# Optimization experiments

Measured on AMD Instinct MI355X. Metric: run time of the kernel, lower is better.

Reference implementation:

```python
import jax, jax.numpy as jnp
import numpy as np

D_IN, D_OUT, RANK = 4096, 4096, 16
ALPHA = 1.0


def setup_inputs() -> dict:
    key = jax.random.key(0)
    ks = jax.random.split(key, 7)
    x = jax.random.normal(ks[0], (8, 2048, D_IN), dtype=jnp.float32)
    W = jax.random.normal(ks[1], (D_IN, D_OUT), dtype=jnp.float32) * (1.0 / np.sqrt(D_IN))
    bias = jax.random.normal(ks[2], (D_OUT,), dtype=jnp.float32) * 0.02
    # he_normal init for a factors; b factors are zeros in the layer, but use small
    # random values so the adapter path contributes numerically to the test.
    a0 = jax.random.normal(ks[3], (D_IN, RANK), dtype=jnp.float32) * np.sqrt(2.0 / D_IN)
    b0 = jax.random.normal(ks[4], (RANK, D_OUT), dtype=jnp.float32) * 0.02
    a1 = jax.random.normal(ks[5], (D_IN, RANK), dtype=jnp.float32) * np.sqrt(2.0 / D_IN)
    b1 = jax.random.normal(ks[6], (RANK, D_OUT), dtype=jnp.float32) * 0.02
    return {"x": x, "W": W, "bias": bias, "a0": a0, "b0": b0, "a1": a1, "b1": b1}


def reference(x, W, bias, a0, b0, a1, b1):
    # LoHA kernel: base + Hadamard product of scaled low-rank factors
    scale = ALPHA / RANK
    p0 = scale * (a0 @ b0)            # [d_in, d_out]
    p1 = scale * (a1 @ b1)            # [d_in, d_out]
    kernel = W + p0 * p1              # [d_in, d_out]
    # Dense call: x @ kernel + bias
    return jnp.einsum('bsd,de->bse', x, kernel) + bias
```

## Files before the change

kernel.cpp:

```cpp
#include <hip/hip_runtime.h>


#define D_IN   4096
#define D_OUT  4096
#define RANKR  16
#define MROWS  16384

typedef __attribute__((ext_vector_type(8))) short short8;
typedef __attribute__((ext_vector_type(4))) float floatx4;

__device__ __forceinline__ unsigned short f2bf(float f) {
    union { float f; unsigned u; } c; c.f = f;
    unsigned r = c.u + 0x7fffu + ((c.u >> 16) & 1u);
    return (unsigned short)(r >> 16);
}

__device__ __forceinline__ void glds16(const void* g, void* l) {
    __builtin_amdgcn_global_load_lds(
        (const __attribute__((address_space(1))) void*)g,
        (__attribute__((address_space(3))) void*)l, 16, 0, 0);
}

__global__ __launch_bounds__(256) void prep(
    const float* __restrict__ W,  const float* __restrict__ a0,
    const float* __restrict__ b0, const float* __restrict__ a1,
    const float* __restrict__ b1, unsigned short* __restrict__ Bt,
    const float* __restrict__ x,  unsigned short* __restrict__ xb) {
    const int tid = threadIdx.x;
    if (blockIdx.x >= 4096) {
        size_t i = ((size_t)(blockIdx.x - 4096) * 256 + tid) * 8;
        const float4* p = (const float4*)(x + i);
        float4 v0 = p[0], v1 = p[1];
        union { unsigned short u[8]; uint4 q; } o;
        o.u[0] = f2bf(v0.x); o.u[1] = f2bf(v0.y);
        o.u[2] = f2bf(v0.z); o.u[3] = f2bf(v0.w);
        o.u[4] = f2bf(v1.x); o.u[5] = f2bf(v1.y);
        o.u[6] = f2bf(v1.z); o.u[7] = f2bf(v1.w);
        *(uint4*)(xb + i) = o.q;
        return;
    }
    __shared__ float Wt[64][65];
    __shared__ float a0t[64][17], a1t[64][17];
    __shared__ float b0t[16][64], b1t[16][64];
    const int k0 = (blockIdx.x & 63) * 64, n0 = (blockIdx.x >> 6) * 64;

    #pragma unroll
    for (int i = 0; i < 16; ++i) {
        int e = i * 256 + tid;
        int kk = e >> 6, nn = e & 63;
        Wt[kk][nn] = W[(size_t)(k0 + kk) * D_OUT + n0 + nn];
    }
    #pragma unroll
    for (int i = 0; i < 4; ++i) {
        int e = i * 256 + tid;
        int kk = e >> 4, r = e & 15;
        a0t[kk][r] = a0[(k0 + kk) * RANKR + r];
        a1t[kk][r] = a1[(k0 + kk) * RANKR + r];
    }
    #pragma unroll
    for (int i = 0; i < 4; ++i) {
        int e = i * 256 + tid;
        int r = e >> 6, nn = e & 63;
        b0t[r][nn] = b0[(size_t)r * D_OUT + n0 + nn];
        b1t[r][nn] = b1[(size_t)r * D_OUT + n0 + nn];
    }
    __syncthreads();

    const float s = 1.0f / 16.0f;
    #pragma unroll 4
    for (int i = 0; i < 16; ++i) {
        int e = i * 256 + tid;
        int kk = e & 63, nn = e >> 6;
        float d0 = 0.f, d1 = 0.f;
        #pragma unroll
        for (int r = 0; r < RANKR; ++r) {
            d0 += a0t[kk][r] * b0t[r][nn];
            d1 += a1t[kk][r] * b1t[r][nn];
        }
        float v = Wt[kk][nn] + (s * d0) * (s * d1);
        Bt[(size_t)(n0 + nn) * D_IN + k0 + kk] = f2bf(v);
    }
}

__global__ __launch_bounds__(256) void gemm_bt(
    const unsigned short* __restrict__ A,
    const unsigned short* __restrict__ B,
    const float* __restrict__ bias,
    float* __restrict__ C) {
    __shared__ __align__(16) unsigned short As[128 * 32];
    __shared__ __align__(16) unsigned short Bs[128 * 32];

    const int tid  = threadIdx.x;
    const int wave = tid >> 6, lane = tid & 63;
    const int quad = lane >> 4, l16 = lane & 15;
    const int m0 = blockIdx.y * 128, n0 = blockIdx.x * 128;
    const int wm = (wave >> 1) * 64, wn = (wave & 1) * 64;
    const int swz = l16 >> 2;

    const unsigned short* Ag = A + (size_t)m0 * D_IN;
    const unsigned short* Bg = B + (size_t)n0 * D_IN;

    floatx4 acc[4][4] = {};

    for (int kt = 0; kt < D_IN; kt += 32) {
        #pragma unroll
        for (int p = 0; p < 2; ++p) {
            int t   = p * 256 + tid;
            int row = t >> 2;
            int cc  = ((t & 3) ^ ((row >> 2) & 3)) * 8;
            unsigned ldsoff = (unsigned)(p * 4096 + wave * 1024);
            glds16(Ag + (size_t)row * D_IN + kt + cc, (char*)As + ldsoff);
            glds16(Bg + (size_t)row * D_IN + kt + cc, (char*)Bs + ldsoff);
        }
        __syncthreads();

        short8 af[4], bf[4];
        #pragma unroll
        for (int mt = 0; mt < 4; ++mt)
            af[mt] = *(const short8*)(As + (wm + mt * 16 + l16) * 32 + (quad ^ swz) * 8);
        #pragma unroll
        for (int nt = 0; nt < 4; ++nt)
            bf[nt] = *(const short8*)(Bs + (wn + nt * 16 + l16) * 32 + (quad ^ swz) * 8);
        #pragma unroll
        for (int mt = 0; mt < 4; ++mt)
            #pragma unroll
            for (int nt = 0; nt < 4; ++nt)
                acc[mt][nt] = __builtin_amdgcn_mfma_f32_16x16x32_bf16(
                    af[mt], bf[nt], acc[mt][nt], 0, 0, 0);
        __syncthreads();
    }

    #pragma unroll
    for (int nt = 0; nt < 4; ++nt) {
        int col = n0 + wn + nt * 16 + l16;
        float bv = bias[col];
        #pragma unroll
        for (int mt = 0; mt < 4; ++mt) {
            int r0 = m0 + wm + mt * 16 + quad * 4;
            #pragma unroll
            for (int r = 0; r < 4; ++r) {
                float v = acc[mt][nt][r] + bv;
                __builtin_nontemporal_store(v, &C[(size_t)(r0 + r) * D_OUT + col]);
            }
        }
    }
}

extern "C" void kernel_launch(void* const* d_in, const int* in_sizes, int n_in,
                              void* d_out, int out_size, void* d_ws, size_t ws_size,
                              hipStream_t stream) {
    const float* x    = (const float*)d_in[0];
    const float* W    = (const float*)d_in[1];
    const float* bias = (const float*)d_in[2];
    const float* a0   = (const float*)d_in[3];
    const float* b0   = (const float*)d_in[4];
    const float* a1   = (const float*)d_in[5];
    const float* b1   = (const float*)d_in[6];
    float* out = (float*)d_out;

    unsigned short* xb = (unsigned short*)d_ws;
    unsigned short* Bt = (unsigned short*)((char*)d_ws + (size_t)MROWS * D_IN * 2);

    prep<<<4096 + (MROWS * (size_t)D_IN) / 2048, 256, 0, stream>>>(
        W, a0, b0, a1, b1, Bt, x, xb);
    gemm_bt<<<dim3(D_OUT / 128, MROWS / 128), 256, 0, stream>>>(xb, Bt, bias, out);
}
```

Before: 1.093 ms.

## Pipeline GEMM with 4-stage LDS ring, 256x256 tiles, and split prep kernels

Rewrites the bf16 GEMM to use 256x256 block tiles with 512 threads, a 4-deep LDS ring buffer fed by async global-to-LDS loads issued three tiles ahead, explicit vmcnt waits, and a single barrier per k-step. It also adds s_setprio around MFMA bursts and a block-index swizzle for L2 locality. The prep kernel is split into a separate x-conversion kernel and a LoHA weight kernel that keeps the a factors in registers and reads b from a transposed LDS layout. The aim is to hide global load latency, raise arithmetic intensity, and cut barrier stalls. The cost is a much larger LDS footprint and more register pressure, which limits occupancy.

```diff
diff --git a/kernel.cpp b/kernel.cpp
--- a/kernel.cpp
+++ b/kernel.cpp
@@ -5,6 +5,7 @@
 #define D_OUT  4096
 #define RANKR  16
 #define MROWS  16384
+#define NTK    128
 
 typedef __attribute__((ext_vector_type(8))) short short8;
 typedef __attribute__((ext_vector_type(4))) float floatx4;
@@ -21,27 +22,26 @@
         (__attribute__((address_space(3))) void*)l, 16, 0, 0);
 }
 
-__global__ __launch_bounds__(256) void prep(
+__global__ __launch_bounds__(256) void cvt_x(const float* __restrict__ x,
+                                             unsigned short* __restrict__ xb) {
+    size_t i = ((size_t)blockIdx.x * 256 + threadIdx.x) * 8;
+    const float4* p = (const float4*)(x + i);
+    float4 v0 = p[0], v1 = p[1];
+    union { unsigned short u[8]; uint4 q; } o;
+    o.u[0] = f2bf(v0.x); o.u[1] = f2bf(v0.y);
+    o.u[2] = f2bf(v0.z); o.u[3] = f2bf(v0.w);
+    o.u[4] = f2bf(v1.x); o.u[5] = f2bf(v1.y);
+    o.u[6] = f2bf(v1.z); o.u[7] = f2bf(v1.w);
+    *(uint4*)(xb + i) = o.q;
+}
+
+__global__ __launch_bounds__(256) void prep_bt(
     const float* __restrict__ W,  const float* __restrict__ a0,
     const float* __restrict__ b0, const float* __restrict__ a1,
-    const float* __restrict__ b1, unsigned short* __restrict__ Bt,
-    const float* __restrict__ x,  unsigned short* __restrict__ xb) {
+    const float* __restrict__ b1, unsigned short* __restrict__ Bt) {
+    __shared__ float Wt[64][65];
+    __shared__ float b0t[64][20], b1t[64][20];
     const int tid = threadIdx.x;
-    if (blockIdx.x >= 4096) {
-        size_t i = ((size_t)(blockIdx.x - 4096) * 256 + tid) * 8;
-        const float4* p = (const float4*)(x + i);
-        float4 v0 = p[0], v1 = p[1];
-        union { unsigned short u[8]; uint4 q; } o;
-        o.u[0] = f2bf(v0.x); o.u[1] = f2bf(v0.y);
-        o.u[2] = f2bf(v0.z); o.u[3] = f2bf(v0.w);
-        o.u[4] = f2bf(v1.x); o.u[5] = f2bf(v1.y);
-        o.u[6] = f2bf(v1.z); o.u[7] = f2bf(v1.w);
-        *(uint4*)(xb + i) = o.q;
-        return;
-    }
-    __shared__ float Wt[64][65];
-    __shared__ float a0t[64][17], a1t[64][17];
-    __shared__ float b0t[16][64], b1t[16][64];
     const int k0 = (blockIdx.x & 63) * 64, n0 = (blockIdx.x >> 6) * 64;
 
     #pragma unroll
@@ -53,90 +53,144 @@
     #pragma unroll
     for (int i = 0; i < 4; ++i) {
         int e = i * 256 + tid;
-        int kk = e >> 4, r = e & 15;
-        a0t[kk][r] = a0[(k0 + kk) * RANKR + r];
-        a1t[kk][r] = a1[(k0 + kk) * RANKR + r];
-    }
-    #pragma unroll
-    for (int i = 0; i < 4; ++i) {
-        int e = i * 256 + tid;
         int r = e >> 6, nn = e & 63;
-        b0t[r][nn] = b0[(size_t)r * D_OUT + n0 + nn];
-        b1t[r][nn] = b1[(size_t)r * D_OUT + n0 + nn];
+        b0t[nn][r] = b0[(size_t)r * D_OUT + n0 + nn];
+        b1t[nn][r] = b1[(size_t)r * D_OUT + n0 + nn];
+    }
+    const int kk = tid & 63;
+    float4 A0[4], A1[4];
+    #pragma unroll
+    for (int c = 0; c < 4; ++c) {
+        A0[c] = *(const float4*)(a0 + (size_t)(k0 + kk) * RANKR + c * 4);
+        A1[c] = *(const float4*)(a1 + (size_t)(k0 + kk) * RANKR + c * 4);
     }
     __syncthreads();
 
-    const float s = 1.0f / 16.0f;
-    #pragma unroll 4
+    const float s2 = 1.0f / 256.0f;
+    #pragma unroll
     for (int i = 0; i < 16; ++i) {
-        int e = i * 256 + tid;
-        int kk = e & 63, nn = e >> 6;
+        int nn = i * 4 + (tid >> 6);
         float d0 = 0.f, d1 = 0.f;
         #pragma unroll
-        for (int r = 0; r < RANKR; ++r) {
-            d0 += a0t[kk][r] * b0t[r][nn];
-            d1 += a1t[kk][r] * b1t[r][nn];
+        for (int c = 0; c < 4; ++c) {
+            float4 bv0 = *(const float4*)&b0t[nn][c * 4];
+            float4 bv1 = *(const float4*)&b1t[nn][c * 4];
+            d0 += A0[c].x * bv0.x + A0[c].y * bv0.y + A0[c].z * bv0.z + A0[c].w * bv0.w;
+            d1 += A1[c].x * bv1.x + A1[c].y * bv1.y + A1[c].z * bv1.z + A1[c].w * bv1.w;
         }
-        float v = Wt[kk][nn] + (s * d0) * (s * d1);
+        float v = Wt[kk][nn] + s2 * d0 * d1;
         Bt[(size_t)(n0 + nn) * D_IN + k0 + kk] = f2bf(v);
     }
 }
 
-__global__ __launch_bounds__(256) void gemm_bt(
+#define STAGE_A(tt) do {                                                      \
+    const int kt_ = (tt) * 32;                                                \
+    unsigned short* const dst_ = &As[(tt) & 3][0];                            \
+    _Pragma("unroll")                                                         \
+    for (int r_ = 0; r_ < 2; ++r_) {                                          \
+      const int e_ = r_ * 512 + tid;                                          \
+      const int row_ = e_ >> 2;                                               \
+      const int cc_ = ((e_ & 3) ^ ((row_ >> 2) & 3)) * 8;                     \
+      glds16(Ag + (size_t)row_ * D_IN + kt_ + cc_,                            \
+             (char*)dst_ + r_ * 8192 + wave * 1024);                          \
+    }                                                                         \
+  } while (0)
+
+#define STAGE_B(tt) do {                                                      \
+    const int kt_ = (tt) * 32;                                                \
+    unsigned short* const dst_ = &Bs[(tt) & 3][0];                            \
+    _Pragma("unroll")                                                         \
+    for (int r_ = 0; r_ < 2; ++r_) {                                          \
+      const int e_ = r_ * 512 + tid;                                          \
+      const int row_ = e_ >> 2;                                               \
+      const int cc_ = ((e_ & 3) ^ ((row_ >> 2) & 3)) * 8;                     \
+      glds16(Bg + (size_t)row_ * D_IN + kt_ + cc_,                            \
+             (char*)dst_ + r_ * 8192 + wave * 1024);                          \
+    }                                                                         \
+  } while (0)
+
+#define TILE(tt, DS) do {                                                     \
+    const unsigned short* const as_ = &As[(tt) & 3][0];                       \
+    const unsigned short* const bs_ = &Bs[(tt) & 3][0];                       \
+    if (DS) STAGE_A((tt) + 3);                                                \
+    short8 bfr[4], afr[4];                                                    \
+    _Pragma("unroll")                                                         \
+    for (int nt_ = 0; nt_ < 4; ++nt_)                                         \
+      bfr[nt_] = *(const short8*)(bs_ + (wn * 64 + nt_ * 16 + l16) * 32 + rc8); \
+    _Pragma("unroll")                                                         \
+    for (int mt_ = 0; mt_ < 4; ++mt_)                                         \
+      afr[mt_] = *(const short8*)(as_ + (wm * 128 + mt_ * 16 + l16) * 32 + rc8); \
+    __builtin_amdgcn_s_setprio(1);                                            \
+    _Pragma("unroll")                                                         \
+    for (int mt_ = 0; mt_ < 4; ++mt_)                                         \
+      _Pragma("unroll")                                                       \
+      for (int nt_ = 0; nt_ < 4; ++nt_)                                       \
+        acc[mt_][nt_] = __builtin_amdgcn_mfma_f32_16x16x32_bf16(              \
+            afr[mt_], bfr[nt_], acc[mt_][nt_], 0, 0, 0);                      \
+    __builtin_amdgcn_s_setprio(0);                                            \
+    if (DS) STAGE_B((tt) + 3);                                                \
+    _Pragma("unroll")                                                         \
+    for (int mt_ = 0; mt_ < 4; ++mt_)                                         \
+      afr[mt_] = *(const short8*)(as_ + (wm * 128 + 64 + mt_ * 16 + l16) * 32 + rc8); \
+    __builtin_amdgcn_s_setprio(1);                                            \
+    _Pragma("unroll")                                                         \
+    for (int mt_ = 0; mt_ < 4; ++mt_)                                         \
+      _Pragma("unroll")                                                       \
+      for (int nt_ = 0; nt_ < 4; ++nt_)                                       \
+        acc[4 + mt_][nt_] = __builtin_amdgcn_mfma_f32_16x16x32_bf16(          \
+            afr[mt_], bfr[nt_], acc[4 + mt_][nt_], 0, 0, 0);                  \
+    __builtin_amdgcn_s_setprio(0);                                            \
+  } while (0)
+
+#define TILE_SYNC(N) do {                                                     \
+    asm volatile("s_waitcnt vmcnt(" #N ")" ::: "memory");                     \
+    __builtin_amdgcn_s_barrier();                                             \
+    asm volatile("" ::: "memory");                                            \
+  } while (0)
+
+__global__ __launch_bounds__(512, 2) void gemm_bt(
     const unsigned short* __restrict__ A,
     const unsigned short* __restrict__ B,
     const float* __restrict__ bias,
     float* __restrict__ C) {
-    __shared__ __align__(16) unsigned short As[128 * 32];
-    __shared__ __align__(16) unsigned short Bs[128 * 32];
+    __shared__ __align__(16) unsigned short As[4][256 * 32];
+    __shared__ __align__(16) unsigned short Bs[4][256 * 32];
 
     const int tid  = threadIdx.x;
     const int wave = tid >> 6, lane = tid & 63;
     const int quad = lane >> 4, l16 = lane & 15;
-    const int m0 = blockIdx.y * 128, n0 = blockIdx.x * 128;
-    const int wm = (wave >> 1) * 64, wn = (wave & 1) * 64;
-    const int swz = l16 >> 2;
+    const int rc8  = (quad ^ (l16 >> 2)) * 8;
+
+    const int bid = blockIdx.y * 16 + blockIdx.x;
+    const int swz = (bid & 7) * 128 + (bid >> 3);
+    const int m0 = (swz >> 4) * 256, n0 = (swz & 15) * 256;
+    const int wm = wave >> 2, wn = wave & 3;
 
     const unsigned short* Ag = A + (size_t)m0 * D_IN;
     const unsigned short* Bg = B + (size_t)n0 * D_IN;
 
-    floatx4 acc[4][4] = {};
-
-    for (int kt = 0; kt < D_IN; kt += 32) {
-        #pragma unroll
-        for (int p = 0; p < 2; ++p) {
-            int t   = p * 256 + tid;
-            int row = t >> 2;
-            int cc  = ((t & 3) ^ ((row >> 2) & 3)) * 8;
-            unsigned ldsoff = (unsigned)(p * 4096 + wave * 1024);
-            glds16(Ag + (size_t)row * D_IN + kt + cc, (char*)As + ldsoff);
-            glds16(Bg + (size_t)row * D_IN + kt + cc, (char*)Bs + ldsoff);
-        }
-        __syncthreads();
-
-        short8 af[4], bf[4];
-        #pragma unroll
-        for (int mt = 0; mt < 4; ++mt)
-            af[mt] = *(const short8*)(As + (wm + mt * 16 + l16) * 32 + (quad ^ swz) * 8);
-        #pragma unroll
-        for (int nt = 0; nt < 4; ++nt)
-            bf[nt] = *(const short8*)(Bs + (wn + nt * 16 + l16) * 32 + (quad ^ swz) * 8);
-        #pragma unroll
-        for (int mt = 0; mt < 4; ++mt)
-            #pragma unroll
-            for (int nt = 0; nt < 4; ++nt)
-                acc[mt][nt] = __builtin_amdgcn_mfma_f32_16x16x32_bf16(
-                    af[mt], bf[nt], acc[mt][nt], 0, 0, 0);
-        __syncthreads();
-    }
+    floatx4 acc[8][4] = {};
+
+    STAGE_A(0); STAGE_B(0);
+    STAGE_A(1); STAGE_B(1);
+    STAGE_A(2); STAGE_B(2);
+    TILE_SYNC(8);
+
+    for (int t = 0; t < NTK - 3; ++t) {
+        TILE(t, 1);
+        TILE_SYNC(8);
+    }
+    TILE(NTK - 3, 0); TILE_SYNC(4);
+    TILE(NTK - 2, 0); TILE_SYNC(0);
+    TILE(NTK - 1, 0);
 
     #pragma unroll
     for (int nt = 0; nt < 4; ++nt) {
-        int col = n0 + wn + nt * 16 + l16;
+        int col = n0 + wn * 64 + nt * 16 + l16;
         float bv = bias[col];
         #pragma unroll
-        for (int mt = 0; mt < 4; ++mt) {
-            int r0 = m0 + wm + mt * 16 + quad * 4;
+        for (int mt = 0; mt < 8; ++mt) {
+            int r0 = m0 + wm * 128 + mt * 16 + quad * 4;
             #pragma unroll
             for (int r = 0; r < 4; ++r) {
                 float v = acc[mt][nt][r] + bv;
@@ -161,7 +215,7 @@
     unsigned short* xb = (unsigned short*)d_ws;
     unsigned short* Bt = (unsigned short*)((char*)d_ws + (size_t)MROWS * D_IN * 2);
 
-    prep<<<4096 + (MROWS * (size_t)D_IN) / 2048, 256, 0, stream>>>(
-        W, a0, b0, a1, b1, Bt, x, xb);
-    gemm_bt<<<dim3(D_OUT / 128, MROWS / 128), 256, 0, stream>>>(xb, Bt, bias, out);
-}
+    cvt_x<<<(MROWS * (size_t)D_IN) / 2048, 256, 0, stream>>>(x, xb);
+    prep_bt<<<4096, 256, 0, stream>>>(W, a0, b0, a1, b1, Bt);
+    gemm_bt<<<dim3(D_OUT / 256, MROWS / 256), 512, 0, stream>>>(xb, Bt, bias, out);
+}
```

Result: slower. 1.157 ms (+5.9%).
